# Optimization experiments

Hardware: AMD Instinct MI355X
Metric: run time of the kernel (lower is better)

## Reference

```python
import jax, jax.numpy as jnp
import numpy as np

B, H, L, D = 2, 16, 2048, 64


def setup_inputs() -> dict:
    key = jax.random.key(0)
    kq, kk, kv = jax.random.split(key, 3)
    return {
        "query": jax.random.normal(kq, (B, H, L, D), dtype=jnp.float32),
        "key": jax.random.normal(kk, (B, H, L, D), dtype=jnp.float32),
        "value": jax.random.normal(kv, (B, H, L, D), dtype=jnp.float32),
        "dhead": D,
        "causal": 1,
    }


def reference(query, key, value, dhead, causal):
    # mode='dhead': muP attention with scale 1/dhead (not 1/sqrt(dhead)).
    # Inputs/outputs in [B, H, L, D] layout (the torch code transposes to
    # [B, L, H, D] for the einsum and transposes back; net layout is the same).
    scale = 1.0 / dhead
    a = jnp.einsum('bhld,bhLd->bhlL', query, key) * scale  # [B,H,L,L]
    if causal:
        seq = a.shape[-1]
        mask = jnp.tril(jnp.ones((seq, seq), dtype=bool))  # [L,L]
        a = jnp.where(mask, a, jnp.float32(-jnp.inf))
    a = jax.nn.softmax(a, axis=-1)
    out = jnp.einsum('bhlL,bhLd->bhld', a, value)  # [B,H,L,D]
    return out
```

## Files before the change

### kernel.cpp

```cpp
#include <hip/hip_runtime.h>

#define BHH 32
#define SEQ 2048
#define DH 64
#define BQ 64
#define BK 64
#define NKT (SEQ / BK)
#define NQB (SEQ / BQ)

typedef __attribute__((ext_vector_type(8))) _Float16 half8_t;
typedef __attribute__((ext_vector_type(4))) _Float16 half4_t;
typedef __attribute__((ext_vector_type(4))) float f32x4;

__device__ __forceinline__ void async_copy16(const void* g, const void* lds) {
    __builtin_amdgcn_global_load_lds(
        (const __attribute__((address_space(1))) unsigned int*)g,
        (__attribute__((address_space(3))) unsigned int*)lds, 16, 0, 0);
}

__global__ __launch_bounds__(256) void prep_k(const float* __restrict__ K,
                                              _Float16* __restrict__ Kf) {
    const int tile = blockIdx.x;
    __shared__ _Float16 lk[64 * 72];
    const int t = threadIdx.x;
    const int row = t >> 2, col0 = (t & 3) * 16;
    const float4* src = (const float4*)(K + (size_t)tile * 4096 + row * 64 + col0);
    #pragma unroll
    for (int q = 0; q < 2; ++q) {
        float4 f0 = src[q * 2], f1 = src[q * 2 + 1];
        half8_t w = { (_Float16)f0.x, (_Float16)f0.y, (_Float16)f0.z, (_Float16)f0.w,
                      (_Float16)f1.x, (_Float16)f1.y, (_Float16)f1.z, (_Float16)f1.w };
        *(half8_t*)&lk[row * 72 + col0 + q * 8] = w;
    }
    __syncthreads();
    const int wave = t >> 6, lane = t & 63, ln15 = lane & 15, quad = lane >> 4;
    #pragma unroll
    for (int p = 0; p < 2; ++p) {
        const int bid = wave * 2 + p, c = bid >> 1, k0 = bid & 1;
        half8_t w = *(const half8_t*)&lk[(c * 16 + ln15) * 72 + k0 * 32 + quad * 8];
        *(half8_t*)&Kf[(size_t)tile * 4096 + bid * 512 + lane * 8] = w;
    }
}

__global__ __launch_bounds__(256) void prep_v(const float* __restrict__ V,
                                              _Float16* __restrict__ Vf) {
    const int tile = blockIdx.x;
    __shared__ _Float16 lv[64 * 76];
    const int t = threadIdx.x;
    const int row = t >> 2, col0 = (t & 3) * 16;
    const float4* src = (const float4*)(V + (size_t)tile * 4096 + row * 64 + col0);
    #pragma unroll
    for (int q = 0; q < 4; ++q) {
        float4 f = src[q];
        half4_t w = { (_Float16)f.x, (_Float16)f.y, (_Float16)f.z, (_Float16)f.w };
        *(half4_t*)&lv[row * 76 + col0 + q * 4] = w;
    }
    __syncthreads();
    const int wave = t >> 6, lane = t & 63, ln15 = lane & 15, quad = lane >> 4;
    #pragma unroll
    for (int p = 0; p < 4; ++p) {
        const int f = wave * 4 + p, cn = f >> 2, c = f & 3;
        half4_t w;
        #pragma unroll
        for (int j = 0; j < 4; ++j)
            w[j] = lv[(c * 16 + quad * 4 + j) * 76 + cn * 16 + ln15];
        *(half4_t*)&Vf[(size_t)tile * 4096 + f * 256 + lane * 4] = w;
    }
}

__global__ __launch_bounds__(128) void fattn_kernel(
        const float* __restrict__ Q, const _Float16* __restrict__ Kf,
        const _Float16* __restrict__ Vf, float* __restrict__ O) {
    const int bh = blockIdx.x & 31;
    const int r = blockIdx.x >> 5, j = r & 7, rnd = r >> 3;
    const int qb = (rnd == 0) ? 31 - j : (rnd == 1) ? 16 + j
                 : (rnd == 2) ? 15 - j : j;
    const int tid  = threadIdx.x;
    const int wave = tid >> 6;
    const int lane = tid & 63;
    const int ln15 = lane & 15;
    const int quad = lane >> 4;

    __shared__ _Float16 ldsK[2][4096];
    __shared__ _Float16 ldsV[2][4096];

    const size_t base = (size_t)bh * SEQ * DH;
    const int q0 = qb * BQ;

    const float qscale = 1.44269504f / 64.0f;
    half8_t qfrag[2][2];
    #pragma unroll
    for (int g = 0; g < 2; ++g) {
        const float* qp = Q + base
            + (size_t)(q0 + (wave * 2 + g) * 16 + ln15) * DH + quad * 8;
        #pragma unroll
        for (int k0 = 0; k0 < 2; ++k0) {
            float4 a = *(const float4*)(qp + k0 * 32);
            float4 b = *(const float4*)(qp + k0 * 32 + 4);
            half8_t w = { (_Float16)(a.x * qscale), (_Float16)(a.y * qscale),
                          (_Float16)(a.z * qscale), (_Float16)(a.w * qscale),
                          (_Float16)(b.x * qscale), (_Float16)(b.y * qscale),
                          (_Float16)(b.z * qscale), (_Float16)(b.w * qscale) };
            qfrag[g][k0] = w;
        }
    }

    f32x4 acc[2][4] = {};
    float l_i[2] = {0.f, 0.f};
    const size_t tb = (size_t)(bh * NKT) * 4096;

    #define STAGE(kt_, b_) do {                                              \
        const size_t toff = tb + (size_t)(kt_) * 4096;                       \
        if (wave == 0) {                                                     \
            _Pragma("unroll")                                                \
            for (int i_ = 0; i_ < 8; ++i_)                                   \
                async_copy16(Kf + toff + i_ * 512 + lane * 8,                \
                             &ldsK[b_][i_ * 512]);                           \
        } else {                                                             \
            _Pragma("unroll")                                                \
            for (int i_ = 0; i_ < 8; ++i_)                                   \
                async_copy16(Vf + toff + i_ * 512 + lane * 8,                \
                             &ldsV[b_][i_ * 512]);                           \
        }                                                                    \
    } while (0)

    const int nkt = qb + 1;
    STAGE(0, 0);
    __syncthreads();

    for (int kt = 0; kt < nkt; ++kt) {
        const _Float16* kvk = ldsK[kt & 1];
        const _Float16* kvv = ldsV[kt & 1];
        if (kt + 1 < nkt) STAGE(kt + 1, (kt + 1) & 1);

        f32x4 st[2][4];
        #pragma unroll
        for (int c = 0; c < 4; ++c) {
            half8_t kf0 = *(const half8_t*)&kvk[(c * 2 + 0) * 512 + lane * 8];
            half8_t kf1 = *(const half8_t*)&kvk[(c * 2 + 1) * 512 + lane * 8];
            #pragma unroll
            for (int g = 0; g < 2; ++g) {
                f32x4 a = {};
                a = __builtin_amdgcn_mfma_f32_16x16x32_f16(kf0, qfrag[g][0], a, 0, 0, 0);
                a = __builtin_amdgcn_mfma_f32_16x16x32_f16(kf1, qfrag[g][1], a, 0, 0, 0);
                st[g][c] = a;
            }
        }

        const int kbase = kt * BK;
        const bool needmask = (kt == qb);
        half4_t pfrag[2][4];
        #pragma unroll
        for (int g = 0; g < 2; ++g) {
            const int rowi = q0 + (wave * 2 + g) * 16 + ln15;
            float psum = 0.f;
            #pragma unroll
            for (int c = 0; c < 4; ++c) {
                #pragma unroll
                for (int rr = 0; rr < 4; ++rr) {
                    float p = __builtin_amdgcn_exp2f(st[g][c][rr]);
                    if (needmask && (kbase + c * 16 + quad * 4 + rr) > rowi) p = 0.f;
                    pfrag[g][c][rr] = (_Float16)p;
                    psum += p;
                }
            }
            psum += __shfl_xor(psum, 16);
            psum += __shfl_xor(psum, 32);
            l_i[g] += psum;
        }

        #pragma unroll
        for (int cn = 0; cn < 4; ++cn) {
            #pragma unroll
            for (int c = 0; c < 4; ++c) {
                half4_t vf = *(const half4_t*)&kvv[(cn * 4 + c) * 256 + lane * 4];
                acc[0][cn] = __builtin_amdgcn_mfma_f32_16x16x16f16(vf, pfrag[0][c], acc[0][cn], 0, 0, 0);
                acc[1][cn] = __builtin_amdgcn_mfma_f32_16x16x16f16(vf, pfrag[1][c], acc[1][cn], 0, 0, 0);
            }
        }
        __syncthreads();
    }

    #pragma unroll
    for (int g = 0; g < 2; ++g) {
        const float rl = 1.0f / l_i[g];
        float* op = O + base + (size_t)(q0 + (wave * 2 + g) * 16 + ln15) * DH;
        #pragma unroll
        for (int cn = 0; cn < 4; ++cn) {
            float4 o;
            o.x = acc[g][cn][0] * rl;
            o.y = acc[g][cn][1] * rl;
            o.z = acc[g][cn][2] * rl;
            o.w = acc[g][cn][3] * rl;
            *(float4*)(op + cn * 16 + quad * 4) = o;
        }
    }
    #undef STAGE
}

extern "C" void kernel_launch(void* const* d_in, const int* in_sizes, int n_in,
                              void* d_out, int out_size, void* d_ws, size_t ws_size,
                              hipStream_t stream) {
    const float* Q = (const float*)d_in[0];
    const float* K = (const float*)d_in[1];
    const float* V = (const float*)d_in[2];
    float* O = (float*)d_out;
    _Float16* Kf = (_Float16*)d_ws;
    _Float16* Vf = Kf + (size_t)BHH * NKT * 4096;
    prep_k<<<BHH * NKT, 256, 0, stream>>>(K, Kf);
    prep_v<<<BHH * NKT, 256, 0, stream>>>(V, Vf);
    fattn_kernel<<<NQB * BHH, 128, 0, stream>>>(Q, Kf, Vf, O);
}
```

Baseline: 136.2 us.

## Merge K/V prep kernels and use four waves per query block in attention

```diff
diff --git a/kernel.cpp b/kernel.cpp
--- a/kernel.cpp
+++ b/kernel.cpp
@@ -7,6 +7,7 @@
 #define BK 64
 #define NKT (SEQ / BK)
 #define NQB (SEQ / BQ)
+#define NT  (BHH * NKT)
 
 typedef __attribute__((ext_vector_type(8))) _Float16 half8_t;
 typedef __attribute__((ext_vector_type(4))) _Float16 half4_t;
@@ -18,57 +19,55 @@
         (__attribute__((address_space(3))) unsigned int*)lds, 16, 0, 0);
 }
 
-__global__ __launch_bounds__(256) void prep_k(const float* __restrict__ K,
-                                              _Float16* __restrict__ Kf) {
-    const int tile = blockIdx.x;
-    __shared__ _Float16 lk[64 * 72];
+__global__ __launch_bounds__(256) void prep_kv(const float* __restrict__ K,
+                                               const float* __restrict__ V,
+                                               _Float16* __restrict__ Kf,
+                                               _Float16* __restrict__ Vf) {
+    __shared__ _Float16 l[64 * 76];
     const int t = threadIdx.x;
+    const int wave = t >> 6, lane = t & 63, ln15 = lane & 15, quad = lane >> 4;
     const int row = t >> 2, col0 = (t & 3) * 16;
-    const float4* src = (const float4*)(K + (size_t)tile * 4096 + row * 64 + col0);
-    #pragma unroll
-    for (int q = 0; q < 2; ++q) {
-        float4 f0 = src[q * 2], f1 = src[q * 2 + 1];
-        half8_t w = { (_Float16)f0.x, (_Float16)f0.y, (_Float16)f0.z, (_Float16)f0.w,
-                      (_Float16)f1.x, (_Float16)f1.y, (_Float16)f1.z, (_Float16)f1.w };
-        *(half8_t*)&lk[row * 72 + col0 + q * 8] = w;
-    }
-    __syncthreads();
-    const int wave = t >> 6, lane = t & 63, ln15 = lane & 15, quad = lane >> 4;
-    #pragma unroll
-    for (int p = 0; p < 2; ++p) {
-        const int bid = wave * 2 + p, c = bid >> 1, k0 = bid & 1;
-        half8_t w = *(const half8_t*)&lk[(c * 16 + ln15) * 72 + k0 * 32 + quad * 8];
-        *(half8_t*)&Kf[(size_t)tile * 4096 + bid * 512 + lane * 8] = w;
-    }
-}
-
-__global__ __launch_bounds__(256) void prep_v(const float* __restrict__ V,
-                                              _Float16* __restrict__ Vf) {
-    const int tile = blockIdx.x;
-    __shared__ _Float16 lv[64 * 76];
-    const int t = threadIdx.x;
-    const int row = t >> 2, col0 = (t & 3) * 16;
-    const float4* src = (const float4*)(V + (size_t)tile * 4096 + row * 64 + col0);
-    #pragma unroll
-    for (int q = 0; q < 4; ++q) {
-        float4 f = src[q];
-        half4_t w = { (_Float16)f.x, (_Float16)f.y, (_Float16)f.z, (_Float16)f.w };
-        *(half4_t*)&lv[row * 76 + col0 + q * 4] = w;
-    }
-    __syncthreads();
-    const int wave = t >> 6, lane = t & 63, ln15 = lane & 15, quad = lane >> 4;
-    #pragma unroll
-    for (int p = 0; p < 4; ++p) {
-        const int f = wave * 4 + p, cn = f >> 2, c = f & 3;
-        half4_t w;
-        #pragma unroll
-        for (int j = 0; j < 4; ++j)
-            w[j] = lv[(c * 16 + quad * 4 + j) * 76 + cn * 16 + ln15];
-        *(half4_t*)&Vf[(size_t)tile * 4096 + f * 256 + lane * 4] = w;
-    }
-}
-
-__global__ __launch_bounds__(128) void fattn_kernel(
+    int b = blockIdx.x;
+
+    if (b < NT) {
+        const float4* src = (const float4*)(K + (size_t)b * 4096 + row * 64 + col0);
+        #pragma unroll
+        for (int q = 0; q < 2; ++q) {
+            float4 f0 = src[q * 2], f1 = src[q * 2 + 1];
+            half8_t w = { (_Float16)f0.x, (_Float16)f0.y, (_Float16)f0.z, (_Float16)f0.w,
+                          (_Float16)f1.x, (_Float16)f1.y, (_Float16)f1.z, (_Float16)f1.w };
+            *(half8_t*)&l[row * 72 + col0 + q * 8] = w;
+        }
+        __syncthreads();
+        #pragma unroll
+        for (int p = 0; p < 2; ++p) {
+            const int bid = wave * 2 + p, c = bid >> 1, k0 = bid & 1;
+            half8_t w = *(const half8_t*)&l[(c * 16 + ln15) * 72 + k0 * 32 + quad * 8];
+            *(half8_t*)&Kf[(size_t)b * 4096 + bid * 512 + lane * 8] = w;
+        }
+    } else {
+        b -= NT;
+        const float4* src = (const float4*)(V + (size_t)b * 4096 + row * 64 + col0);
+        #pragma unroll
+        for (int q = 0; q < 4; ++q) {
+            float4 f = src[q];
+            half4_t w = { (_Float16)f.x, (_Float16)f.y, (_Float16)f.z, (_Float16)f.w };
+            *(half4_t*)&l[row * 76 + col0 + q * 4] = w;
+        }
+        __syncthreads();
+        #pragma unroll
+        for (int p = 0; p < 4; ++p) {
+            const int f = wave * 4 + p, cn = f >> 2, c = f & 3;
+            half4_t w;
+            #pragma unroll
+            for (int j = 0; j < 4; ++j)
+                w[j] = l[(c * 16 + quad * 4 + j) * 76 + cn * 16 + ln15];
+            *(half4_t*)&Vf[(size_t)b * 4096 + f * 256 + lane * 4] = w;
+        }
+    }
+}
+
+__global__ __launch_bounds__(256) void fattn_kernel(
         const float* __restrict__ Q, const _Float16* __restrict__ Kf,
         const _Float16* __restrict__ Vf, float* __restrict__ O) {
     const int bh = blockIdx.x & 31;
@@ -85,42 +84,40 @@
     __shared__ _Float16 ldsV[2][4096];
 
     const size_t base = (size_t)bh * SEQ * DH;
-    const int q0 = qb * BQ;
+    const int q0   = qb * BQ;
+    const int qrow = q0 + wave * 16;
 
     const float qscale = 1.44269504f / 64.0f;
-    half8_t qfrag[2][2];
-    #pragma unroll
-    for (int g = 0; g < 2; ++g) {
-        const float* qp = Q + base
-            + (size_t)(q0 + (wave * 2 + g) * 16 + ln15) * DH + quad * 8;
+    half8_t qfrag[2];
+    {
+        const float* qp = Q + base + (size_t)(qrow + ln15) * DH + quad * 8;
         #pragma unroll
         for (int k0 = 0; k0 < 2; ++k0) {
             float4 a = *(const float4*)(qp + k0 * 32);
             float4 b = *(const float4*)(qp + k0 * 32 + 4);
-            half8_t w = { (_Float16)(a.x * qscale), (_Float16)(a.y * qscale),
-                          (_Float16)(a.z * qscale), (_Float16)(a.w * qscale),
-                          (_Float16)(b.x * qscale), (_Float16)(b.y * qscale),
-                          (_Float16)(b.z * qscale), (_Float16)(b.w * qscale) };
-            qfrag[g][k0] = w;
-        }
-    }
-
-    f32x4 acc[2][4] = {};
-    float l_i[2] = {0.f, 0.f};
+            qfrag[k0] = (half8_t){
+                (_Float16)(a.x * qscale), (_Float16)(a.y * qscale),
+                (_Float16)(a.z * qscale), (_Float16)(a.w * qscale),
+                (_Float16)(b.x * qscale), (_Float16)(b.y * qscale),
+                (_Float16)(b.z * qscale), (_Float16)(b.w * qscale) };
+        }
+    }
+
+    f32x4 acc[4] = {};
+    float l_i = 0.f;
     const size_t tb = (size_t)(bh * NKT) * 4096;
 
     #define STAGE(kt_, b_) do {                                              \
         const size_t toff = tb + (size_t)(kt_) * 4096;                       \
-        if (wave == 0) {                                                     \
-            _Pragma("unroll")                                                \
-            for (int i_ = 0; i_ < 8; ++i_)                                   \
-                async_copy16(Kf + toff + i_ * 512 + lane * 8,                \
-                             &ldsK[b_][i_ * 512]);                           \
-        } else {                                                             \
-            _Pragma("unroll")                                                \
-            for (int i_ = 0; i_ < 8; ++i_)                                   \
-                async_copy16(Vf + toff + i_ * 512 + lane * 8,                \
-                             &ldsV[b_][i_ * 512]);                           \
+        _Pragma("unroll")                                                    \
+        for (int i_ = 0; i_ < 4; ++i_) {                                     \
+            const int bid_ = wave * 4 + i_;                                  \
+            if (bid_ < 8)                                                    \
+                async_copy16(Kf + toff + bid_ * 512 + lane * 8,              \
+                             &ldsK[b_][bid_ * 512]);                         \
+            else                                                             \
+                async_copy16(Vf + toff + (bid_ - 8) * 512 + lane * 8,        \
+                             &ldsV[b_][(bid_ - 8) * 512]);                   \
         }                                                                    \
     } while (0)
 
@@ -133,65 +130,57 @@
         const _Float16* kvv = ldsV[kt & 1];
         if (kt + 1 < nkt) STAGE(kt + 1, (kt + 1) & 1);
 
-        f32x4 st[2][4];
+        f32x4 st[4];
         #pragma unroll
         for (int c = 0; c < 4; ++c) {
             half8_t kf0 = *(const half8_t*)&kvk[(c * 2 + 0) * 512 + lane * 8];
             half8_t kf1 = *(const half8_t*)&kvk[(c * 2 + 1) * 512 + lane * 8];
-            #pragma unroll
-            for (int g = 0; g < 2; ++g) {
-                f32x4 a = {};
-                a = __builtin_amdgcn_mfma_f32_16x16x32_f16(kf0, qfrag[g][0], a, 0, 0, 0);
-                a = __builtin_amdgcn_mfma_f32_16x16x32_f16(kf1, qfrag[g][1], a, 0, 0, 0);
-                st[g][c] = a;
-            }
+            f32x4 a = {};
+            a = __builtin_amdgcn_mfma_f32_16x16x32_f16(kf0, qfrag[0], a, 0, 0, 0);
+            a = __builtin_amdgcn_mfma_f32_16x16x32_f16(kf1, qfrag[1], a, 0, 0, 0);
+            st[c] = a;
         }
 
         const int kbase = kt * BK;
         const bool needmask = (kt == qb);
-        half4_t pfrag[2][4];
-        #pragma unroll
-        for (int g = 0; g < 2; ++g) {
-            const int rowi = q0 + (wave * 2 + g) * 16 + ln15;
-            float psum = 0.f;
+        const int rowi = qrow + ln15;
+        half4_t pfrag[4];
+        float psum = 0.f;
+        #pragma unroll
+        for (int c = 0; c < 4; ++c) {
             #pragma unroll
-            for (int c = 0; c < 4; ++c) {
-                #pragma unroll
-                for (int rr = 0; rr < 4; ++rr) {
-                    float p = __builtin_amdgcn_exp2f(st[g][c][rr]);
-                    if (needmask && (kbase + c * 16 + quad * 4 + rr) > rowi) p = 0.f;
-                    pfrag[g][c][rr] = (_Float16)p;
-                    psum += p;
-                }
+            for (int rr = 0; rr < 4; ++rr) {
+                float v = __builtin_amdgcn_exp2f(st[c][rr]);
+                if (needmask && (kbase + c * 16 + quad * 4 + rr) > rowi) v = 0.f;
+                pfrag[c][rr] = (_Float16)v;
+                psum += v;
             }
-            psum += __shfl_xor(psum, 16);
-            psum += __shfl_xor(psum, 32);
-            l_i[g] += psum;
-        }
+        }
+        psum += __shfl_xor(psum, 16);
+        psum += __shfl_xor(psum, 32);
+        l_i += psum;
 
         #pragma unroll
         for (int cn = 0; cn < 4; ++cn) {
             #pragma unroll
             for (int c = 0; c < 4; ++c) {
                 half4_t vf = *(const half4_t*)&kvv[(cn * 4 + c) * 256 + lane * 4];
-                acc[0][cn] = __builtin_amdgcn_mfma_f32_16x16x16f16(vf, pfrag[0][c], acc[0][cn], 0, 0, 0);
-                acc[1][cn] = __builtin_amdgcn_mfma_f32_16x16x16f16(vf, pfrag[1][c], acc[1][cn], 0, 0, 0);
+                acc[cn] = __builtin_amdgcn_mfma_f32_16x16x16f16(vf, pfrag[c], acc[cn], 0, 0, 0);
             }
         }
         __syncthreads();
     }
 
-    #pragma unroll
-    for (int g = 0; g < 2; ++g) {
-        const float rl = 1.0f / l_i[g];
-        float* op = O + base + (size_t)(q0 + (wave * 2 + g) * 16 + ln15) * DH;
+    {
+        const float rl = 1.0f / l_i;
+        float* op = O + base + (size_t)(qrow + ln15) * DH;
         #pragma unroll
         for (int cn = 0; cn < 4; ++cn) {
             float4 o;
-            o.x = acc[g][cn][0] * rl;
-            o.y = acc[g][cn][1] * rl;
-            o.z = acc[g][cn][2] * rl;
-            o.w = acc[g][cn][3] * rl;
+            o.x = acc[cn][0] * rl;
+            o.y = acc[cn][1] * rl;
+            o.z = acc[cn][2] * rl;
+            o.w = acc[cn][3] * rl;
             *(float4*)(op + cn * 16 + quad * 4) = o;
         }
     }
@@ -206,8 +195,7 @@
     const float* V = (const float*)d_in[2];
     float* O = (float*)d_out;
     _Float16* Kf = (_Float16*)d_ws;
-    _Float16* Vf = Kf + (size_t)BHH * NKT * 4096;
-    prep_k<<<BHH * NKT, 256, 0, stream>>>(K, Kf);
-    prep_v<<<BHH * NKT, 256, 0, stream>>>(V, Vf);
-    fattn_kernel<<<NQB * BHH, 128, 0, stream>>>(Q, Kf, Vf, O);
-}
+    _Float16* Vf = Kf + (size_t)NT * 4096;
+    prep_kv<<<2 * NT, 256, 0, stream>>>(K, V, Kf, Vf);
+    fattn_kernel<<<NQB * BHH, 256, 0, stream>>>(Q, Kf, Vf, O);
+}
```

Result: faster. 129.7 us (-4.8%).
